# Performance work log

Hardware: AMD Instinct MI355X
Metric: run time of the kernel (lower is better)

The kernel has to match this reference:

```python
import jax, jax.numpy as jnp
import numpy as np

N_EMBD = 64
N_HEAD = 8
HEAD_SIZE = N_EMBD // N_HEAD  # 8
BLOCK_SIZE = 64
B = 4096
SCALE = N_EMBD ** (-0.5)  # NOTE: source scales by C**-0.5 with C=n_embd, not head_size
EPS = 1e-5


def setup_inputs() -> dict:
    key = jax.random.key(0)
    ks = jax.random.split(key, 12)
    s = 0.02
    return {
        "x": jax.random.normal(ks[0], (B, BLOCK_SIZE, N_EMBD), jnp.float32),
        # per-head q/k/v projections packed as [C, H, hs] (no bias in source)
        "Wq": jax.random.normal(ks[1], (N_EMBD, N_HEAD, HEAD_SIZE), jnp.float32) * s,
        "Wk": jax.random.normal(ks[2], (N_EMBD, N_HEAD, HEAD_SIZE), jnp.float32) * s,
        "Wv": jax.random.normal(ks[3], (N_EMBD, N_HEAD, HEAD_SIZE), jnp.float32) * s,
        "Wo": jax.random.normal(ks[4], (N_EMBD, N_EMBD), jnp.float32) * s,
        "bo": jnp.zeros((N_EMBD,), jnp.float32),
        "W1": jax.random.normal(ks[5], (N_EMBD, 4 * N_EMBD), jnp.float32) * s,
        "b1": jnp.zeros((4 * N_EMBD,), jnp.float32),
        "W2": jax.random.normal(ks[6], (4 * N_EMBD, N_EMBD), jnp.float32) * s,
        "b2": jnp.zeros((N_EMBD,), jnp.float32),
        "g1": jnp.ones((N_EMBD,), jnp.float32),
        "be1": jnp.zeros((N_EMBD,), jnp.float32),
        "g2": jnp.ones((N_EMBD,), jnp.float32),
        "be2": jnp.zeros((N_EMBD,), jnp.float32),
    }


def _layernorm(x, g, b):
    mu = jnp.mean(x, axis=-1, keepdims=True)
    var = jnp.mean(jnp.square(x - mu), axis=-1, keepdims=True)
    return (x - mu) * jax.lax.rsqrt(var + EPS) * g + b


def reference(x, Wq, Wk, Wv, Wo, bo, W1, b1, W2, b2, g1, be1, g2, be2):
    Bb, T, C = x.shape
    # --- multi-head causal self-attention (dropout = identity in eval) ---
    h = _layernorm(x, g1, be1)
    q = jnp.einsum('btc,chd->bhtd', h, Wq)
    k = jnp.einsum('btc,chd->bhtd', h, Wk)
    v = jnp.einsum('btc,chd->bhtd', h, Wv)
    wei = jnp.einsum('bhtd,bhsd->bhts', q, k) * SCALE
    mask = jnp.tril(jnp.ones((T, T), dtype=bool))
    wei = jnp.where(mask, wei, -jnp.inf)
    wei = jax.nn.softmax(wei, axis=-1)
    attn = jnp.einsum('bhts,bhsd->bhtd', wei, v)
    attn = attn.transpose(0, 2, 1, 3).reshape(Bb, T, C)  # concat heads
    x = x + attn @ Wo + bo
    # --- feed-forward ---
    h2 = _layernorm(x, g2, be2)
    ff = jax.nn.relu(h2 @ W1 + b1) @ W2 + b2
    return x + ff
```

## Files before the change

### kernel.cpp

```cpp
#include <hip/hip_runtime.h>
#include <hip/hip_bf16.h>


typedef __attribute__((ext_vector_type(8))) short short8;
typedef __attribute__((ext_vector_type(4))) float f32x4;

#if __has_builtin(__builtin_amdgcn_exp2f)
#define EXP2F(x) __builtin_amdgcn_exp2f(x)
#else
#define EXP2F(x) __expf((x) * 0.69314718056f)
#endif
#if __has_builtin(__builtin_amdgcn_rcpf)
#define RCPF(x) __builtin_amdgcn_rcpf(x)
#else
#define RCPF(x) (1.0f / (x))
#endif

#define ST  72
#define STU 136
#define OH  0
#define OKK 4608
#define OV  9216
#define OP  13896
#define OU  4608
#define NSH 18504

__device__ __forceinline__ short f2bf(float f) {
    unsigned int u = __float_as_uint(f);
    u += 0x7fffu + ((u >> 16) & 1u);
    return (short)(u >> 16);
}
__device__ __forceinline__ unsigned pk2(float a, float b) {
    float2 t; t.x = a; t.y = b;
    __hip_bfloat162 h = __float22bfloat162_rn(t);
    unsigned u; __builtin_memcpy(&u, &h, 4); return u;
}
__device__ __forceinline__ f32x4 mfma16(short8 a, short8 b, f32x4 c) {
    return __builtin_amdgcn_mfma_f32_16x16x32_bf16(a, b, c, 0, 0, 0);
}

__global__ __launch_bounds__(64) void prepack_kernel(
    const float* __restrict__ Wq, const float* __restrict__ Wk,
    const float* __restrict__ Wv, const float* __restrict__ Wo,
    const float* __restrict__ W1, const float* __restrict__ W2,
    short* __restrict__ ws)
{
    int gid = blockIdx.x * 64 + threadIdx.x;
    int lane = gid & 63;
    int fid  = gid >> 6;
    int quad = lane >> 4, nn = lane & 15;
    short8 o;
    if (fid < 24) {
        int tile = fid >> 1, ks = fid & 1;
        const float* Ws = (tile < 4) ? Wq : ((tile < 8) ? Wk : Wv);
        float scale = (tile < 4) ? 0.18033688011f : 1.0f;
        int col = (tile & 3) * 16 + nn;
#pragma unroll
        for (int j = 0; j < 8; ++j)
            o[j] = f2bf(Ws[(ks * 32 + quad * 8 + j) * 64 + col] * scale);
    } else if (fid < 32) {
        int idx = fid - 24, nt = idx >> 1, ks = idx & 1;
#pragma unroll
        for (int j = 0; j < 8; ++j)
            o[j] = f2bf(Wo[(ks * 32 + quad * 8 + j) * 64 + nt * 16 + nn]);
    } else if (fid < 64) {
        int idx = fid - 32, c = idx >> 3, tile = (idx >> 1) & 3, ks = idx & 1;
#pragma unroll
        for (int j = 0; j < 8; ++j)
            o[j] = f2bf(W1[(ks * 32 + quad * 8 + j) * 256 + c * 64 + tile * 16 + nn]);
    } else {
        int idx = fid - 64, c = idx >> 3, nt = (idx >> 1) & 3, ks = idx & 1;
#pragma unroll
        for (int j = 0; j < 8; ++j)
            o[j] = f2bf(W2[(c * 64 + ks * 32 + quad * 8 + j) * 64 + nt * 16 + nn]);
    }
    *(short8*)(ws + (size_t)gid * 8) = o;
}

__global__ __launch_bounds__(256, 4) void block_kernel(
    const float* __restrict__ x,
    const float* __restrict__ bo,
    const float* __restrict__ b1,
    const float* __restrict__ b2,
    const float* __restrict__ g1, const float* __restrict__ be1,
    const float* __restrict__ g2, const float* __restrict__ be2,
    const short8* __restrict__ WB,
    float* __restrict__ out)
{
    __shared__ short sm[NSH];
    const int tid  = threadIdx.x;
    const int wv   = tid >> 6;
    const int lane = tid & 63;
    const int quad = lane >> 4;
    const int nn   = lane & 15;
    const int t_my = wv * 16 + nn;
    const int b    = blockIdx.x;
    const float* xb = x + (size_t)b * 4096;
    const f32x4 zf = {0.f, 0.f, 0.f, 0.f};
    const short8 z8 = {0, 0, 0, 0, 0, 0, 0, 0};

    if (tid < ST) sm[OV + 64 * ST + tid] = (short)0x3F80;
    float xr[16];
    float gv[4], bv[4];
#pragma unroll
    for (int nt = 0; nt < 4; ++nt) { gv[nt] = g1[nt * 16 + nn]; bv[nt] = be1[nt * 16 + nn]; }
#pragma unroll
    for (int nt = 0; nt < 4; ++nt)
#pragma unroll
        for (int r = 0; r < 4; ++r)
            xr[nt * 4 + r] = xb[(wv * 16 + quad * 4 + r) * 64 + nt * 16 + nn];
#pragma unroll
    for (int r = 0; r < 4; ++r) {
        float s1 = 0.f, s2 = 0.f;
#pragma unroll
        for (int nt = 0; nt < 4; ++nt) { float v = xr[nt * 4 + r]; s1 += v; s2 += v * v; }
        s1 += __shfl_xor(s1, 1); s1 += __shfl_xor(s1, 2); s1 += __shfl_xor(s1, 4); s1 += __shfl_xor(s1, 8);
        s2 += __shfl_xor(s2, 1); s2 += __shfl_xor(s2, 2); s2 += __shfl_xor(s2, 4); s2 += __shfl_xor(s2, 8);
        float mu = s1 * 0.015625f;
        float rstd = rsqrtf(s2 * 0.015625f - mu * mu + 1e-5f);
        int base = OH + (wv * 16 + quad * 4 + r) * ST + nn;
        float h0 = (xr[0 + r]  - mu) * rstd * gv[0] + bv[0];
        float h1 = (xr[4 + r]  - mu) * rstd * gv[1] + bv[1];
        float h2 = (xr[8 + r]  - mu) * rstd * gv[2] + bv[2];
        float h3 = (xr[12 + r] - mu) * rstd * gv[3] + bv[3];
        unsigned pA = pk2(h0, h1), pB = pk2(h2, h3);
        sm[base +  0] = (short)pA;
        sm[base + 16] = (short)(pA >> 16);
        sm[base + 32] = (short)pB;
        sm[base + 48] = (short)(pB >> 16);
    }
    __syncthreads();

    unsigned qp[8];
    {
        const short8 wk0 = WB[(size_t)((4 + wv) * 2 + 0) * 64 + lane];
        const short8 wk1 = WB[(size_t)((4 + wv) * 2 + 1) * 64 + lane];
        const short8 wv0 = WB[(size_t)((8 + wv) * 2 + 0) * 64 + lane];
        const short8 wv1 = WB[(size_t)((8 + wv) * 2 + 1) * 64 + lane];
#pragma unroll
        for (int rt = 0; rt < 4; ++rt) {
            short8 hA = *(const short8*)&sm[OH + (rt * 16 + nn) * ST + quad * 8];
            short8 hB = *(const short8*)&sm[OH + (rt * 16 + nn) * ST + 32 + quad * 8];
            f32x4 ka = mfma16(wk0, hA, zf); ka = mfma16(wk1, hB, ka);
            uint2 w1; w1.x = pk2(ka[0], ka[1]); w1.y = pk2(ka[2], ka[3]);
            *(uint2*)&sm[OKK + (rt * 16 + nn) * ST + wv * 16 + quad * 4] = w1;
            f32x4 va = mfma16(hA, wv0, zf); va = mfma16(hB, wv1, va);
            uint2 w2; w2.x = pk2(va[0], va[1]); w2.y = pk2(va[2], va[3]);
            *(uint2*)&sm[OV + (wv * 16 + nn) * ST + rt * 16 + quad * 4] = w2;
        }
        short8 hf0 = *(const short8*)&sm[OH + t_my * ST + quad * 8];
        short8 hf1 = *(const short8*)&sm[OH + t_my * ST + 32 + quad * 8];
#pragma unroll
        for (int jt = 0; jt < 4; ++jt) {
            f32x4 a = mfma16(WB[(size_t)(jt * 2 + 0) * 64 + lane], hf0, zf);
            a = mfma16(WB[(size_t)(jt * 2 + 1) * 64 + lane], hf1, a);
            qp[jt * 2 + 0] = pk2(a[0], a[1]);
            qp[jt * 2 + 1] = pk2(a[2], a[3]);
        }
    }
    __syncthreads();

    const bool keep0 = (quad * 4 + 0) <= nn, keep1 = (quad * 4 + 1) <= nn;
    const bool keep2 = (quad * 4 + 2) <= nn, keep3 = (quad * 4 + 3) <= nn;
    const int arow_base = (nn < 8) ? nn : 64;
    const int arow_step = (nn < 8) ? 8 : 0;
    const int nks = (wv < 2) ? 1 : 2;
    const int zhi = nks * 2;
    for (int mt = wv + 1; mt < zhi; ++mt) {
        uint2 w; w.x = 0u; w.y = 0u;
        *(uint2*)&sm[OP + t_my * ST + mt * 16 + quad * 4] = w;
    }
    short8 bq8[8];
#pragma unroll
    for (int h = 0; h < 8; ++h) {
        int qsA = ((h & 1) * 2) * 16 + nn, qsB = qsA + 16;
        int qi = (h >> 1) * 2;
        union { unsigned u[4]; short8 s; } bb;
        bb.u[0] = __shfl(qp[qi + 0], qsA);
        bb.u[1] = __shfl(qp[qi + 1], qsA);
        bb.u[2] = __shfl(qp[qi + 0], qsB);
        bb.u[3] = __shfl(qp[qi + 1], qsB);
        bq8[h] = bb.s;
    }
#pragma unroll
    for (int h = 0; h < 8; ++h) {
        const short8 bq = bq8[h];
#pragma unroll
        for (int mt = 0; mt < 4; ++mt) {
            if (mt <= wv) {
                short8 ak = z8;
                if (quad == 0) ak = *(const short8*)&sm[OKK + (mt * 16 + nn) * ST + h * 8];
                f32x4 s = mfma16(ak, bq, zf);
                float e0 = EXP2F(s[0]), e1 = EXP2F(s[1]), e2 = EXP2F(s[2]), e3 = EXP2F(s[3]);
                if (mt == wv) {
                    e0 = keep0 ? e0 : 0.f; e1 = keep1 ? e1 : 0.f;
                    e2 = keep2 ? e2 : 0.f; e3 = keep3 ? e3 : 0.f;
                }
                uint2 w; w.x = pk2(e0, e1); w.y = pk2(e2, e3);
                *(uint2*)&sm[OP + t_my * ST + mt * 16 + quad * 4] = w;
            }
        }
        const int arow = arow_base + h * arow_step;
        f32x4 pv = zf;
#pragma unroll
        for (int ks = 0; ks < 2; ++ks) {
            if (ks < nks) {
                short8 av = *(const short8*)&sm[OV + arow * ST + ks * 32 + quad * 8];
                short8 bp = *(const short8*)&sm[OP + t_my * ST + ks * 32 + quad * 8];
                pv = mfma16(av, bp, pv);
            }
        }
        float denom = __shfl(pv[0], 32 + nn);
        float rd = RCPF(denom);
        if (quad < 2) {
            uint2 w; w.x = pk2(pv[0] * rd, pv[1] * rd); w.y = pk2(pv[2] * rd, pv[3] * rd);
            *(uint2*)&sm[OH + t_my * ST + h * 8 + quad * 4] = w;
        }
    }

    {
        short8 aa0 = *(const short8*)&sm[OH + t_my * ST + quad * 8];
        short8 aa1 = *(const short8*)&sm[OH + t_my * ST + 32 + quad * 8];
#pragma unroll
        for (int nt = 0; nt < 4; ++nt) {
            f32x4 oa = mfma16(aa0, WB[(size_t)(24 + nt * 2 + 0) * 64 + lane], zf);
            oa = mfma16(aa1, WB[(size_t)(24 + nt * 2 + 1) * 64 + lane], oa);
            float bov = bo[nt * 16 + nn];
#pragma unroll
            for (int r = 0; r < 4; ++r) xr[nt * 4 + r] += oa[r] + bov;
        }
    }
#pragma unroll
    for (int nt = 0; nt < 4; ++nt) { gv[nt] = g2[nt * 16 + nn]; bv[nt] = be2[nt * 16 + nn]; }
#pragma unroll
    for (int r = 0; r < 4; ++r) {
        float s1 = 0.f, s2 = 0.f;
#pragma unroll
        for (int nt = 0; nt < 4; ++nt) { float v = xr[nt * 4 + r]; s1 += v; s2 += v * v; }
        s1 += __shfl_xor(s1, 1); s1 += __shfl_xor(s1, 2); s1 += __shfl_xor(s1, 4); s1 += __shfl_xor(s1, 8);
        s2 += __shfl_xor(s2, 1); s2 += __shfl_xor(s2, 2); s2 += __shfl_xor(s2, 4); s2 += __shfl_xor(s2, 8);
        float mu = s1 * 0.015625f;
        float rstd = rsqrtf(s2 * 0.015625f - mu * mu + 1e-5f);
        int base = OP + (wv * 16 + quad * 4 + r) * ST + nn;
        float h0 = (xr[0 + r]  - mu) * rstd * gv[0] + bv[0];
        float h1 = (xr[4 + r]  - mu) * rstd * gv[1] + bv[1];
        float h2 = (xr[8 + r]  - mu) * rstd * gv[2] + bv[2];
        float h3 = (xr[12 + r] - mu) * rstd * gv[3] + bv[3];
        unsigned pA = pk2(h0, h1), pB = pk2(h2, h3);
        sm[base +  0] = (short)pA;
        sm[base + 16] = (short)(pA >> 16);
        sm[base + 32] = (short)pB;
        sm[base + 48] = (short)(pB >> 16);
    }
    __syncthreads();

    short8 h2r[4][2];
#pragma unroll
    for (int rt = 0; rt < 4; ++rt) {
        h2r[rt][0] = *(const short8*)&sm[OP + (rt * 16 + nn) * ST + quad * 8];
        h2r[rt][1] = *(const short8*)&sm[OP + (rt * 16 + nn) * ST + 32 + quad * 8];
    }
    f32x4 fa[4];
#pragma unroll
    for (int rt = 0; rt < 4; ++rt) fa[rt] = zf;
#pragma unroll
    for (int c = 0; c < 2; ++c) {
#pragma unroll
        for (int g = 0; g < 2; ++g) {
            int gc = c * 8 + wv * 2 + g;
            int fid = 32 + (gc >> 2) * 8 + (gc & 3) * 2;
            short8 wf0 = WB[(size_t)fid * 64 + lane];
            short8 wf1 = WB[(size_t)(fid + 1) * 64 + lane];
            const float4 bb = *(const float4*)&b1[gc * 16 + quad * 4];
#pragma unroll
            for (int rt = 0; rt < 4; ++rt) {
                f32x4 u = mfma16(wf0, h2r[rt][0], zf);
                u = mfma16(wf1, h2r[rt][1], u);
                float u0 = fmaxf(u[0] + bb.x, 0.f), u1 = fmaxf(u[1] + bb.y, 0.f);
                float u2 = fmaxf(u[2] + bb.z, 0.f), u3 = fmaxf(u[3] + bb.w, 0.f);
                uint2 w; w.x = pk2(u0, u1); w.y = pk2(u2, u3);
                *(uint2*)&sm[OU + (rt * 16 + nn) * STU + (wv * 2 + g) * 16 + quad * 4] = w;
            }
        }
        __syncthreads();
#pragma unroll
        for (int kl = 0; kl < 4; ++kl) {
            int fidb = 64 + (c * 2 + (kl >> 1)) * 8 + wv * 2 + (kl & 1);
            short8 w2f = WB[(size_t)fidb * 64 + lane];
#pragma unroll
            for (int rt = 0; rt < 4; ++rt) {
                short8 au = *(const short8*)&sm[OU + (rt * 16 + nn) * STU + kl * 32 + quad * 8];
                fa[rt] = mfma16(au, w2f, fa[rt]);
            }
        }
        if (c == 0) __syncthreads();
    }
    {
        float* yr = (wv < 2) ? (float*)sm : (float*)(sm + OP);
        const int ycol = (wv & 1) * 16 + nn;
#pragma unroll
        for (int rt = 0; rt < 4; ++rt)
#pragma unroll
            for (int r = 0; r < 4; ++r)
                yr[(rt * 16 + quad * 4 + r) * 34 + ycol] = fa[rt][r];
    }
    __syncthreads();

    float* ob = out + (size_t)b * 4096;
    const float* yA = (const float*)sm;
    const float* yB = (const float*)(sm + OP);
#pragma unroll
    for (int nt = 0; nt < 4; ++nt) {
        const float* ys = (nt < 2) ? yA : yB;
        float b2v = b2[nt * 16 + nn];
#pragma unroll
        for (int r = 0; r < 4; ++r) {
            float yv = ys[(wv * 16 + quad * 4 + r) * 34 + (nt & 1) * 16 + nn];
            ob[(wv * 16 + quad * 4 + r) * 64 + nt * 16 + nn] = xr[nt * 4 + r] + yv + b2v;
        }
    }
}

extern "C" void kernel_launch(void* const* d_in, const int* in_sizes, int n_in,
                              void* d_out, int out_size, void* d_ws, size_t ws_size,
                              hipStream_t stream) {
    const float* x   = (const float*)d_in[0];
    const float* Wq  = (const float*)d_in[1];
    const float* Wk  = (const float*)d_in[2];
    const float* Wv  = (const float*)d_in[3];
    const float* Wo  = (const float*)d_in[4];
    const float* bo  = (const float*)d_in[5];
    const float* W1  = (const float*)d_in[6];
    const float* b1  = (const float*)d_in[7];
    const float* W2  = (const float*)d_in[8];
    const float* b2  = (const float*)d_in[9];
    const float* g1  = (const float*)d_in[10];
    const float* be1 = (const float*)d_in[11];
    const float* g2  = (const float*)d_in[12];
    const float* be2 = (const float*)d_in[13];
    short* ws = (short*)d_ws;
    prepack_kernel<<<dim3(96), dim3(64), 0, stream>>>(Wq, Wk, Wv, Wo, W1, W2, ws);
    const int nb = in_sizes[0] / 4096;
    block_kernel<<<dim3(nb), dim3(256), 0, stream>>>(
        x, bo, b1, b2, g1, be1, g2, be2, (const short8*)ws, (float*)d_out);
}
```

Before: 193.4 us.

## Split block work across eight waves with head and row-tile partitioning

The block grows from 256 to 512 threads. The second group of four waves takes the V projection, half of the Q heads, half of the attention heads (using a separate probability buffer in shared memory), and half of the FFN row tiles. LayerNorm, the output projection and the final store stay on the first four waves. The aim is more wave-level parallelism per batch element to hide latency, at the cost of more shared memory, an extra barrier, and idle waves during the serial phases.

```diff
diff --git a/kernel.cpp b/kernel.cpp
--- a/kernel.cpp
+++ b/kernel.cpp
@@ -23,7 +23,7 @@
 #define OV  9216
 #define OP  13896
 #define OU  4608
-#define NSH 18504
+#define NSH 23112
 
 __device__ __forceinline__ short f2bf(float f) {
     unsigned int u = __float_as_uint(f);
@@ -77,7 +77,7 @@
     *(short8*)(ws + (size_t)gid * 8) = o;
 }
 
-__global__ __launch_bounds__(256, 4) void block_kernel(
+__global__ __launch_bounds__(512, 4) void block_kernel(
     const float* __restrict__ x,
     const float* __restrict__ bo,
     const float* __restrict__ b1,
@@ -89,7 +89,9 @@
 {
     __shared__ short sm[NSH];
     const int tid  = threadIdx.x;
-    const int wv   = tid >> 6;
+    const int w    = tid >> 6;
+    const int wv   = w & 3;
+    const int hh   = w >> 2;
     const int lane = tid & 63;
     const int quad = lane >> 4;
     const int nn   = lane & 15;
@@ -102,60 +104,71 @@
     if (tid < ST) sm[OV + 64 * ST + tid] = (short)0x3F80;
     float xr[16];
     float gv[4], bv[4];
-#pragma unroll
-    for (int nt = 0; nt < 4; ++nt) { gv[nt] = g1[nt * 16 + nn]; bv[nt] = be1[nt * 16 + nn]; }
-#pragma unroll
-    for (int nt = 0; nt < 4; ++nt)
-#pragma unroll
-        for (int r = 0; r < 4; ++r)
-            xr[nt * 4 + r] = xb[(wv * 16 + quad * 4 + r) * 64 + nt * 16 + nn];
-#pragma unroll
-    for (int r = 0; r < 4; ++r) {
-        float s1 = 0.f, s2 = 0.f;
-#pragma unroll
-        for (int nt = 0; nt < 4; ++nt) { float v = xr[nt * 4 + r]; s1 += v; s2 += v * v; }
-        s1 += __shfl_xor(s1, 1); s1 += __shfl_xor(s1, 2); s1 += __shfl_xor(s1, 4); s1 += __shfl_xor(s1, 8);
-        s2 += __shfl_xor(s2, 1); s2 += __shfl_xor(s2, 2); s2 += __shfl_xor(s2, 4); s2 += __shfl_xor(s2, 8);
-        float mu = s1 * 0.015625f;
-        float rstd = rsqrtf(s2 * 0.015625f - mu * mu + 1e-5f);
-        int base = OH + (wv * 16 + quad * 4 + r) * ST + nn;
-        float h0 = (xr[0 + r]  - mu) * rstd * gv[0] + bv[0];
-        float h1 = (xr[4 + r]  - mu) * rstd * gv[1] + bv[1];
-        float h2 = (xr[8 + r]  - mu) * rstd * gv[2] + bv[2];
-        float h3 = (xr[12 + r] - mu) * rstd * gv[3] + bv[3];
-        unsigned pA = pk2(h0, h1), pB = pk2(h2, h3);
-        sm[base +  0] = (short)pA;
-        sm[base + 16] = (short)(pA >> 16);
-        sm[base + 32] = (short)pB;
-        sm[base + 48] = (short)(pB >> 16);
-    }
-    __syncthreads();
-
-    unsigned qp[8];
+    if (w < 4) {
+#pragma unroll
+        for (int nt = 0; nt < 4; ++nt) { gv[nt] = g1[nt * 16 + nn]; bv[nt] = be1[nt * 16 + nn]; }
+#pragma unroll
+        for (int nt = 0; nt < 4; ++nt)
+#pragma unroll
+            for (int r = 0; r < 4; ++r)
+                xr[nt * 4 + r] = xb[(wv * 16 + quad * 4 + r) * 64 + nt * 16 + nn];
+#pragma unroll
+        for (int r = 0; r < 4; ++r) {
+            float s1 = 0.f, s2 = 0.f;
+#pragma unroll
+            for (int nt = 0; nt < 4; ++nt) { float v = xr[nt * 4 + r]; s1 += v; s2 += v * v; }
+            s1 += __shfl_xor(s1, 1); s1 += __shfl_xor(s1, 2); s1 += __shfl_xor(s1, 4); s1 += __shfl_xor(s1, 8);
+            s2 += __shfl_xor(s2, 1); s2 += __shfl_xor(s2, 2); s2 += __shfl_xor(s2, 4); s2 += __shfl_xor(s2, 8);
+            float mu = s1 * 0.015625f;
+            float rstd = rsqrtf(s2 * 0.015625f - mu * mu + 1e-5f);
+            int base = OH + (wv * 16 + quad * 4 + r) * ST + nn;
+            float h0 = (xr[0 + r]  - mu) * rstd * gv[0] + bv[0];
+            float h1 = (xr[4 + r]  - mu) * rstd * gv[1] + bv[1];
+            float h2 = (xr[8 + r]  - mu) * rstd * gv[2] + bv[2];
+            float h3 = (xr[12 + r] - mu) * rstd * gv[3] + bv[3];
+            unsigned pA = pk2(h0, h1), pB = pk2(h2, h3);
+            sm[base +  0] = (short)pA;
+            sm[base + 16] = (short)(pA >> 16);
+            sm[base + 32] = (short)pB;
+            sm[base + 48] = (short)(pB >> 16);
+        }
+    }
+    __syncthreads();
+
+    unsigned qp[4];
     {
-        const short8 wk0 = WB[(size_t)((4 + wv) * 2 + 0) * 64 + lane];
-        const short8 wk1 = WB[(size_t)((4 + wv) * 2 + 1) * 64 + lane];
-        const short8 wv0 = WB[(size_t)((8 + wv) * 2 + 0) * 64 + lane];
-        const short8 wv1 = WB[(size_t)((8 + wv) * 2 + 1) * 64 + lane];
-#pragma unroll
-        for (int rt = 0; rt < 4; ++rt) {
-            short8 hA = *(const short8*)&sm[OH + (rt * 16 + nn) * ST + quad * 8];
-            short8 hB = *(const short8*)&sm[OH + (rt * 16 + nn) * ST + 32 + quad * 8];
-            f32x4 ka = mfma16(wk0, hA, zf); ka = mfma16(wk1, hB, ka);
-            uint2 w1; w1.x = pk2(ka[0], ka[1]); w1.y = pk2(ka[2], ka[3]);
-            *(uint2*)&sm[OKK + (rt * 16 + nn) * ST + wv * 16 + quad * 4] = w1;
-            f32x4 va = mfma16(hA, wv0, zf); va = mfma16(hB, wv1, va);
-            uint2 w2; w2.x = pk2(va[0], va[1]); w2.y = pk2(va[2], va[3]);
-            *(uint2*)&sm[OV + (wv * 16 + nn) * ST + rt * 16 + quad * 4] = w2;
+        if (hh == 0) {
+            const short8 wk0 = WB[(size_t)((4 + wv) * 2 + 0) * 64 + lane];
+            const short8 wk1 = WB[(size_t)((4 + wv) * 2 + 1) * 64 + lane];
+#pragma unroll
+            for (int rt = 0; rt < 4; ++rt) {
+                short8 hA = *(const short8*)&sm[OH + (rt * 16 + nn) * ST + quad * 8];
+                short8 hB = *(const short8*)&sm[OH + (rt * 16 + nn) * ST + 32 + quad * 8];
+                f32x4 ka = mfma16(wk0, hA, zf); ka = mfma16(wk1, hB, ka);
+                uint2 w1; w1.x = pk2(ka[0], ka[1]); w1.y = pk2(ka[2], ka[3]);
+                *(uint2*)&sm[OKK + (rt * 16 + nn) * ST + wv * 16 + quad * 4] = w1;
+            }
+        } else {
+            const short8 wv0 = WB[(size_t)((8 + wv) * 2 + 0) * 64 + lane];
+            const short8 wv1 = WB[(size_t)((8 + wv) * 2 + 1) * 64 + lane];
+#pragma unroll
+            for (int rt = 0; rt < 4; ++rt) {
+                short8 hA = *(const short8*)&sm[OH + (rt * 16 + nn) * ST + quad * 8];
+                short8 hB = *(const short8*)&sm[OH + (rt * 16 + nn) * ST + 32 + quad * 8];
+                f32x4 va = mfma16(hA, wv0, zf); va = mfma16(hB, wv1, va);
+                uint2 w2; w2.x = pk2(va[0], va[1]); w2.y = pk2(va[2], va[3]);
+                *(uint2*)&sm[OV + (wv * 16 + nn) * ST + rt * 16 + quad * 4] = w2;
+            }
         }
         short8 hf0 = *(const short8*)&sm[OH + t_my * ST + quad * 8];
         short8 hf1 = *(const short8*)&sm[OH + t_my * ST + 32 + quad * 8];
 #pragma unroll
-        for (int jt = 0; jt < 4; ++jt) {
+        for (int j = 0; j < 2; ++j) {
+            int jt = hh * 2 + j;
             f32x4 a = mfma16(WB[(size_t)(jt * 2 + 0) * 64 + lane], hf0, zf);
             a = mfma16(WB[(size_t)(jt * 2 + 1) * 64 + lane], hf1, a);
-            qp[jt * 2 + 0] = pk2(a[0], a[1]);
-            qp[jt * 2 + 1] = pk2(a[2], a[3]);
+            qp[j * 2 + 0] = pk2(a[0], a[1]);
+            qp[j * 2 + 1] = pk2(a[2], a[3]);
         }
     }
     __syncthreads();
@@ -166,25 +179,27 @@
     const int arow_step = (nn < 8) ? 8 : 0;
     const int nks = (wv < 2) ? 1 : 2;
     const int zhi = nks * 2;
+    const int OPw = OP + hh * 4608;
     for (int mt = wv + 1; mt < zhi; ++mt) {
-        uint2 w; w.x = 0u; w.y = 0u;
-        *(uint2*)&sm[OP + t_my * ST + mt * 16 + quad * 4] = w;
-    }
-    short8 bq8[8];
-#pragma unroll
-    for (int h = 0; h < 8; ++h) {
-        int qsA = ((h & 1) * 2) * 16 + nn, qsB = qsA + 16;
-        int qi = (h >> 1) * 2;
+        uint2 wz; wz.x = 0u; wz.y = 0u;
+        *(uint2*)&sm[OPw + t_my * ST + mt * 16 + quad * 4] = wz;
+    }
+    short8 bq4[4];
+#pragma unroll
+    for (int lh = 0; lh < 4; ++lh) {
+        int qsA = ((lh & 1) * 2) * 16 + nn, qsB = qsA + 16;
+        int qi = (lh >> 1) * 2;
         union { unsigned u[4]; short8 s; } bb;
         bb.u[0] = __shfl(qp[qi + 0], qsA);
         bb.u[1] = __shfl(qp[qi + 1], qsA);
         bb.u[2] = __shfl(qp[qi + 0], qsB);
         bb.u[3] = __shfl(qp[qi + 1], qsB);
-        bq8[h] = bb.s;
-    }
-#pragma unroll
-    for (int h = 0; h < 8; ++h) {
-        const short8 bq = bq8[h];
+        bq4[lh] = bb.s;
+    }
+#pragma unroll
+    for (int lh = 0; lh < 4; ++lh) {
+        const int h = hh * 4 + lh;
+        const short8 bq = bq4[lh];
 #pragma unroll
         for (int mt = 0; mt < 4; ++mt) {
             if (mt <= wv) {
@@ -196,8 +211,8 @@
                     e0 = keep0 ? e0 : 0.f; e1 = keep1 ? e1 : 0.f;
                     e2 = keep2 ? e2 : 0.f; e3 = keep3 ? e3 : 0.f;
                 }
-                uint2 w; w.x = pk2(e0, e1); w.y = pk2(e2, e3);
-                *(uint2*)&sm[OP + t_my * ST + mt * 16 + quad * 4] = w;
+                uint2 wp; wp.x = pk2(e0, e1); wp.y = pk2(e2, e3);
+                *(uint2*)&sm[OPw + t_my * ST + mt * 16 + quad * 4] = wp;
             }
         }
         const int arow = arow_base + h * arow_step;
@@ -206,19 +221,21 @@
         for (int ks = 0; ks < 2; ++ks) {
             if (ks < nks) {
                 short8 av = *(const short8*)&sm[OV + arow * ST + ks * 32 + quad * 8];
-                short8 bp = *(const short8*)&sm[OP + t_my * ST + ks * 32 + quad * 8];
+                short8 bp = *(const short8*)&sm[OPw + t_my * ST + ks * 32 + quad * 8];
                 pv = mfma16(av, bp, pv);
             }
         }
         float denom = __shfl(pv[0], 32 + nn);
         float rd = RCPF(denom);
         if (quad < 2) {
-            uint2 w; w.x = pk2(pv[0] * rd, pv[1] * rd); w.y = pk2(pv[2] * rd, pv[3] * rd);
-            *(uint2*)&sm[OH + t_my * ST + h * 8 + quad * 4] = w;
-        }
-    }
-
-    {
+            uint2 wa;
+            wa.x = pk2(pv[0] * rd, pv[1] * rd); wa.y = pk2(pv[2] * rd, pv[3] * rd);
+            *(uint2*)&sm[OH + t_my * ST + h * 8 + quad * 4] = wa;
+        }
+    }
+    __syncthreads();
+
+    if (w < 4) {
         short8 aa0 = *(const short8*)&sm[OH + t_my * ST + quad * 8];
         short8 aa1 = *(const short8*)&sm[OH + t_my * ST + 32 + quad * 8];
 #pragma unroll
@@ -229,28 +246,28 @@
 #pragma unroll
             for (int r = 0; r < 4; ++r) xr[nt * 4 + r] += oa[r] + bov;
         }
-    }
-#pragma unroll
-    for (int nt = 0; nt < 4; ++nt) { gv[nt] = g2[nt * 16 + nn]; bv[nt] = be2[nt * 16 + nn]; }
-#pragma unroll
-    for (int r = 0; r < 4; ++r) {
-        float s1 = 0.f, s2 = 0.f;
-#pragma unroll
-        for (int nt = 0; nt < 4; ++nt) { float v = xr[nt * 4 + r]; s1 += v; s2 += v * v; }
-        s1 += __shfl_xor(s1, 1); s1 += __shfl_xor(s1, 2); s1 += __shfl_xor(s1, 4); s1 += __shfl_xor(s1, 8);
-        s2 += __shfl_xor(s2, 1); s2 += __shfl_xor(s2, 2); s2 += __shfl_xor(s2, 4); s2 += __shfl_xor(s2, 8);
-        float mu = s1 * 0.015625f;
-        float rstd = rsqrtf(s2 * 0.015625f - mu * mu + 1e-5f);
-        int base = OP + (wv * 16 + quad * 4 + r) * ST + nn;
-        float h0 = (xr[0 + r]  - mu) * rstd * gv[0] + bv[0];
-        float h1 = (xr[4 + r]  - mu) * rstd * gv[1] + bv[1];
-        float h2 = (xr[8 + r]  - mu) * rstd * gv[2] + bv[2];
-        float h3 = (xr[12 + r] - mu) * rstd * gv[3] + bv[3];
-        unsigned pA = pk2(h0, h1), pB = pk2(h2, h3);
-        sm[base +  0] = (short)pA;
-        sm[base + 16] = (short)(pA >> 16);
-        sm[base + 32] = (short)pB;
-        sm[base + 48] = (short)(pB >> 16);
+#pragma unroll
+        for (int nt = 0; nt < 4; ++nt) { gv[nt] = g2[nt * 16 + nn]; bv[nt] = be2[nt * 16 + nn]; }
+#pragma unroll
+        for (int r = 0; r < 4; ++r) {
+            float s1 = 0.f, s2 = 0.f;
+#pragma unroll
+            for (int nt = 0; nt < 4; ++nt) { float v = xr[nt * 4 + r]; s1 += v; s2 += v * v; }
+            s1 += __shfl_xor(s1, 1); s1 += __shfl_xor(s1, 2); s1 += __shfl_xor(s1, 4); s1 += __shfl_xor(s1, 8);
+            s2 += __shfl_xor(s2, 1); s2 += __shfl_xor(s2, 2); s2 += __shfl_xor(s2, 4); s2 += __shfl_xor(s2, 8);
+            float mu = s1 * 0.015625f;
+            float rstd = rsqrtf(s2 * 0.015625f - mu * mu + 1e-5f);
+            int base = OP + (wv * 16 + quad * 4 + r) * ST + nn;
+            float h0 = (xr[0 + r]  - mu) * rstd * gv[0] + bv[0];
+            float h1 = (xr[4 + r]  - mu) * rstd * gv[1] + bv[1];
+            float h2 = (xr[8 + r]  - mu) * rstd * gv[2] + bv[2];
+            float h3 = (xr[12 + r] - mu) * rstd * gv[3] + bv[3];
+            unsigned pA = pk2(h0, h1), pB = pk2(h2, h3);
+            sm[base +  0] = (short)pA;
+            sm[base + 16] = (short)(pA >> 16);
+            sm[base + 32] = (short)pB;
+            sm[base + 48] = (short)(pB >> 16);
+        }
     }
     __syncthreads();
 
@@ -260,14 +277,12 @@
         h2r[rt][0] = *(const short8*)&sm[OP + (rt * 16 + nn) * ST + quad * 8];
         h2r[rt][1] = *(const short8*)&sm[OP + (rt * 16 + nn) * ST + 32 + quad * 8];
     }
-    f32x4 fa[4];
-#pragma unroll
-    for (int rt = 0; rt < 4; ++rt) fa[rt] = zf;
+    f32x4 fa[2];
+    fa[0] = zf; fa[1] = zf;
 #pragma unroll
     for (int c = 0; c < 2; ++c) {
-#pragma unroll
-        for (int g = 0; g < 2; ++g) {
-            int gc = c * 8 + wv * 2 + g;
+        {
+            int gc = c * 8 + w;
             int fid = 32 + (gc >> 2) * 8 + (gc & 3) * 2;
             short8 wf0 = WB[(size_t)fid * 64 + lane];
             short8 wf1 = WB[(size_t)(fid + 1) * 64 + lane];
@@ -278,8 +293,8 @@
                 u = mfma16(wf1, h2r[rt][1], u);
                 float u0 = fmaxf(u[0] + bb.x, 0.f), u1 = fmaxf(u[1] + bb.y, 0.f);
                 float u2 = fmaxf(u[2] + bb.z, 0.f), u3 = fmaxf(u[3] + bb.w, 0.f);
-                uint2 w; w.x = pk2(u0, u1); w.y = pk2(u2, u3);
-                *(uint2*)&sm[OU + (rt * 16 + nn) * STU + (wv * 2 + g) * 16 + quad * 4] = w;
+                uint2 wu; wu.x = pk2(u0, u1); wu.y = pk2(u2, u3);
+                *(uint2*)&sm[OU + (rt * 16 + nn) * STU + w * 16 + quad * 4] = wu;
             }
         }
         __syncthreads();
@@ -288,9 +303,10 @@
             int fidb = 64 + (c * 2 + (kl >> 1)) * 8 + wv * 2 + (kl & 1);
             short8 w2f = WB[(size_t)fidb * 64 + lane];
 #pragma unroll
-            for (int rt = 0; rt < 4; ++rt) {
+            for (int lrt = 0; lrt < 2; ++lrt) {
+                int rt = hh * 2 + lrt;
                 short8 au = *(const short8*)&sm[OU + (rt * 16 + nn) * STU + kl * 32 + quad * 8];
-                fa[rt] = mfma16(au, w2f, fa[rt]);
+                fa[lrt] = mfma16(au, w2f, fa[lrt]);
             }
         }
         if (c == 0) __syncthreads();
@@ -299,24 +315,28 @@
         float* yr = (wv < 2) ? (float*)sm : (float*)(sm + OP);
         const int ycol = (wv & 1) * 16 + nn;
 #pragma unroll
-        for (int rt = 0; rt < 4; ++rt)
+        for (int lrt = 0; lrt < 2; ++lrt) {
+            int rt = hh * 2 + lrt;
 #pragma unroll
             for (int r = 0; r < 4; ++r)
-                yr[(rt * 16 + quad * 4 + r) * 34 + ycol] = fa[rt][r];
-    }
-    __syncthreads();
-
-    float* ob = out + (size_t)b * 4096;
-    const float* yA = (const float*)sm;
-    const float* yB = (const float*)(sm + OP);
-#pragma unroll
-    for (int nt = 0; nt < 4; ++nt) {
-        const float* ys = (nt < 2) ? yA : yB;
-        float b2v = b2[nt * 16 + nn];
-#pragma unroll
-        for (int r = 0; r < 4; ++r) {
-            float yv = ys[(wv * 16 + quad * 4 + r) * 34 + (nt & 1) * 16 + nn];
-            ob[(wv * 16 + quad * 4 + r) * 64 + nt * 16 + nn] = xr[nt * 4 + r] + yv + b2v;
+                yr[(rt * 16 + quad * 4 + r) * 34 + ycol] = fa[lrt][r];
+        }
+    }
+    __syncthreads();
+
+    if (w < 4) {
+        float* ob = out + (size_t)b * 4096;
+        const float* yA = (const float*)sm;
+        const float* yB = (const float*)(sm + OP);
+#pragma unroll
+        for (int nt = 0; nt < 4; ++nt) {
+            const float* ys = (nt < 2) ? yA : yB;
+            float b2v = b2[nt * 16 + nn];
+#pragma unroll
+            for (int r = 0; r < 4; ++r) {
+                float yv = ys[(wv * 16 + quad * 4 + r) * 34 + (nt & 1) * 16 + nn];
+                ob[(wv * 16 + quad * 4 + r) * 64 + nt * 16 + nn] = xr[nt * 4 + r] + yv + b2v;
+            }
         }
     }
 }
@@ -341,6 +361,6 @@
     short* ws = (short*)d_ws;
     prepack_kernel<<<dim3(96), dim3(64), 0, stream>>>(Wq, Wk, Wv, Wo, W1, W2, ws);
     const int nb = in_sizes[0] / 4096;
-    block_kernel<<<dim3(nb), dim3(256), 0, stream>>>(
+    block_kernel<<<dim3(nb), dim3(512), 0, stream>>>(
         x, bo, b1, b2, g1, be1, g2, be2, (const short8*)ws, (float*)d_out);
 }
```

Result: slower. 211.8 us (+9.5%).
